# Performance work log

Hardware: AMD Instinct MI355X
Metric: run time of the kernel (lower is better)

## Reference

```python
import jax, jax.numpy as jnp
import numpy as np
import math

H, HKV, HD, HID = 32, 8, 128, 4096
ROPE_BASE = 10000.0

def rotate_half(x):
    x1, x2 = jnp.split(x, 2, axis=-1)
    return jnp.concatenate([-x2, x1], axis=-1)

def setup_inputs() -> dict:
    key = jax.random.key(0)
    ks = jax.random.split(key, 6)
    B, S = 1, 2048
    s = 0.02
    return {
        "hidden_states": jax.random.normal(ks[0], (B, S, HID), jnp.float32),
        "position_ids": jnp.arange(S, dtype=jnp.int64)[None, :].repeat(B, axis=0),
        # weights stored as [in, out] (transpose of torch Linear weight)
        "wq": jax.random.normal(ks[1], (HID, H * HD), jnp.float32) * s,
        "wk": jax.random.normal(ks[2], (HID, HKV * HD), jnp.float32) * s,
        "wv": jax.random.normal(ks[3], (HID, HKV * HD), jnp.float32) * s,
        "wo": jax.random.normal(ks[4], (H * HD, HID), jnp.float32) * s,
    }

def reference(hidden_states, position_ids, wq, wk, wv, wo):
    B, S, _ = hidden_states.shape
    g = H // HKV
    # projections
    q = (hidden_states @ wq).reshape(B, S, H, HD).transpose(0, 2, 1, 3)    # [B,H,S,D]
    k = (hidden_states @ wk).reshape(B, S, HKV, HD).transpose(0, 2, 1, 3)  # [B,Hkv,S,D]
    v = (hidden_states @ wv).reshape(B, S, HKV, HD).transpose(0, 2, 1, 3)
    # rotary embedding
    inv_freq = 1.0 / (ROPE_BASE ** (jnp.arange(0, HD, 2, dtype=jnp.float32) / HD))
    t = position_ids.astype(jnp.float32)                      # [B,S]
    freqs = t[..., None] * inv_freq[None, None, :]            # [B,S,D/2]
    emb = jnp.concatenate([freqs, freqs], axis=-1)            # [B,S,D]
    cos = jnp.cos(emb)[:, None, :, :]                         # [B,1,S,D]
    sin = jnp.sin(emb)[:, None, :, :]
    q = q * cos + rotate_half(q) * sin
    k = k * cos + rotate_half(k) * sin
    # GQA expansion (repeat_interleave over head dim)
    k = jnp.repeat(k, g, axis=1)                              # [B,H,S,D]
    v = jnpp_repeat(v, g) if False else jnp.repeat(v, g, axis=1)
    scale = 1.0 / math.sqrt(HD)
    scores = jnp.einsum('bhqd,bhkd->bhqk', q, k) * scale      # [B,H,S,S]
    causal = jnp.triu(jnp.full((S, S), -jnp.inf, jnp.float32), k=1)
    scores = scores + causal[None, None]
    attn = jax.nn.softmax(scores.astype(jnp.float32), axis=-1).astype(q.dtype)
    out = jnp.einsum('bhqk,bhkd->bhqd', attn, v)              # [B,H,S,D]
    out = out.transpose(0, 2, 1, 3).reshape(B, S, H * HD)
    return out @ wo
```

## Files before the change

### kernel.cpp

```cpp
#include <hip/hip_runtime.h>
#include <stdint.h>

#define DHEAD 128
#define DMODEL 4096
#define NQKV 6144
#define SEQLEN 2048

typedef __attribute__((ext_vector_type(8))) short bh8;
typedef __attribute__((ext_vector_type(4))) short bh4;
typedef __attribute__((ext_vector_type(4))) float f32x4;

__device__ __forceinline__ short f2bf(float f) {
  union { float f; unsigned u; } x; x.f = f;
  unsigned r = x.u + 0x7FFFu + ((x.u >> 16) & 1u);
  return (short)(r >> 16);
}
__device__ __forceinline__ float bf2f(short s) {
  union { unsigned u; float f; } x; x.u = ((unsigned)(unsigned short)s) << 16;
  return x.f;
}
__device__ __forceinline__ void async_cp16(const void* g, void* l) {
  __builtin_amdgcn_global_load_lds((const __attribute__((address_space(1))) void*)g,
                                   (__attribute__((address_space(3))) void*)l, 16, 0, 0);
}

#define BARRIER() do { asm volatile("" ::: "memory"); __builtin_amdgcn_s_barrier(); asm volatile("" ::: "memory"); } while (0)
#define LGKM0() asm volatile("s_waitcnt lgkmcnt(0)" ::: "memory")

__global__ void cvt_bf16_kernel(const float* __restrict__ src, short* __restrict__ dst, int n) {
  int idx = (blockIdx.x * blockDim.x + threadIdx.x) * 4;
  if (idx >= n) return;
  float4 v = *(const float4*)(src + idx);
  bh4 o;
  o.x = f2bf(v.x); o.y = f2bf(v.y); o.z = f2bf(v.z); o.w = f2bf(v.w);
  *(bh4*)(dst + idx) = o;
}

__global__ void cvt_t_kernel(const float* __restrict__ src, short* __restrict__ dst, int K, int N) {
  __shared__ float tile[32][33];
  int bx = blockIdx.x * 32;
  int by = blockIdx.y * 32;
  int tx = threadIdx.x, ty = threadIdx.y;
  for (int j = 0; j < 4; j++)
    tile[ty + 8 * j][tx] = src[(size_t)(by + ty + 8 * j) * N + bx + tx];
  __syncthreads();
  for (int j = 0; j < 4; j++)
    dst[(size_t)(bx + ty + 8 * j) * K + by + tx] = f2bf(tile[tx][ty + 8 * j]);
}

__global__ void vtrans_kernel(const short* __restrict__ qkv, short* __restrict__ VT) {
  __shared__ short tile[32][33];
  int bx = blockIdx.x * 32;
  int by = blockIdx.y * 32;
  int tx = threadIdx.x, ty = threadIdx.y;
  for (int j = 0; j < 4; j++)
    tile[ty + 8 * j][tx] = qkv[(size_t)(by + ty + 8 * j) * NQKV + 5120 + bx + tx];
  __syncthreads();
  for (int j = 0; j < 4; j++)
    VT[(size_t)(bx + ty + 8 * j) * 2048 + by + tx] = tile[tx][ty + 8 * j];
}

template <typename OutT>
__global__ __launch_bounds__(512, 2) void gemm256(const short* __restrict__ A, const short* __restrict__ Bt,
                                                  OutT* __restrict__ C, int M, int N, int K) {
  __shared__ __align__(16) short lds[2][2][256 * 64];
  const int tid = threadIdx.x;
  const int lane = tid & 63, w = tid >> 6;
  const int l15 = lane & 15, q4 = lane >> 4;
  const int m0 = blockIdx.y * 256, n0 = blockIdx.x * 256;
  const int wm = (w >> 2) * 128, wn = (w & 3) * 64;
  const int NT = K >> 6;

  char* const ldsBase = (char*)lds;

  const int srow = tid >> 3;
  const int scol = ((tid & 7) * 8) ^ ((tid & 32) ? 16 : 0);
  const short* const Asrc = A + (size_t)m0 * K + scol;
  const short* const Bsrc = Bt + (size_t)n0 * K + scol;

  auto stageA = [&](int buf, int h, int kt) {
    char* d = ldsBase + buf * 65536 + h * 16384 + tid * 16;
    const short* s = Asrc + (size_t)(h * 128 + srow) * K + kt * 64;
    async_cp16(s, d);
    async_cp16(s + (size_t)64 * K, d + 8192);
  };
  auto stageB = [&](int buf, int h, int kt) {
    char* d = ldsBase + buf * 65536 + 32768 + h * 16384 + tid * 16;
    const short* s = Bsrc + (size_t)(h * 128 + srow) * K + kt * 64;
    async_cp16(s, d);
    async_cp16(s + (size_t)64 * K, d + 8192);
  };

  const int flip = (l15 & 4) ? 32 : 0;
  const int rdA = (wm + l15) * 128;
  const int rdB = (wn + l15) * 128;
  const int rk0 = (q4 * 16) ^ flip;
  const int rk1 = (64 + q4 * 16) ^ flip;

  f32x4 acc[8][4] = {};
  bh8 af[4][2], bfr[4][2];

  stageA(0, 0, 0); stageA(0, 1, 0); stageB(0, 0, 0); stageB(0, 1, 0);
  stageB(1, 0, 1); stageB(1, 1, 1); stageA(1, 0, 1);
  asm volatile("s_waitcnt vmcnt(6)" ::: "memory");
  BARRIER();

  for (int t = 0; t < NT; ++t) {
    const int buf = t & 1;
    char* const Ar = ldsBase + buf * 65536;
    char* const Br = Ar + 32768;

#pragma unroll
    for (int i = 0; i < 4; i++) {
      af[i][0] = *(const bh8*)(Ar + rdA + i * 2048 + rk0);
      af[i][1] = *(const bh8*)(Ar + rdA + i * 2048 + rk1);
      bfr[i][0] = *(const bh8*)(Br + rdB + i * 2048 + rk0);
      bfr[i][1] = *(const bh8*)(Br + rdB + i * 2048 + rk1);
    }
    if (t + 1 < NT) stageA(buf ^ 1, 1, t + 1);
    BARRIER();
    LGKM0();
    __builtin_amdgcn_s_setprio(1);
#pragma unroll
    for (int i = 0; i < 4; i++)
#pragma unroll
      for (int j = 0; j < 2; j++) {
        acc[i][j] = __builtin_amdgcn_mfma_f32_16x16x32_bf16(af[i][0], bfr[j][0], acc[i][j], 0, 0, 0);
        acc[i][j] = __builtin_amdgcn_mfma_f32_16x16x32_bf16(af[i][1], bfr[j][1], acc[i][j], 0, 0, 0);
      }
    __builtin_amdgcn_s_setprio(0);
    BARRIER();

    if (t + 2 < NT) stageB(buf, 0, t + 2);
    BARRIER();
    __builtin_amdgcn_s_setprio(1);
#pragma unroll
    for (int i = 0; i < 4; i++)
#pragma unroll
      for (int j = 2; j < 4; j++) {
        acc[i][j] = __builtin_amdgcn_mfma_f32_16x16x32_bf16(af[i][0], bfr[j][0], acc[i][j], 0, 0, 0);
        acc[i][j] = __builtin_amdgcn_mfma_f32_16x16x32_bf16(af[i][1], bfr[j][1], acc[i][j], 0, 0, 0);
      }
    __builtin_amdgcn_s_setprio(0);
    BARRIER();

#pragma unroll
    for (int i = 0; i < 4; i++) {
      af[i][0] = *(const bh8*)(Ar + rdA + 8192 + i * 2048 + rk0);
      af[i][1] = *(const bh8*)(Ar + rdA + 8192 + i * 2048 + rk1);
    }
    if (t + 2 < NT) stageB(buf, 1, t + 2);
    BARRIER();
    LGKM0();
    __builtin_amdgcn_s_setprio(1);
#pragma unroll
    for (int i = 0; i < 4; i++)
#pragma unroll
      for (int j = 0; j < 2; j++) {
        acc[4 + i][j] = __builtin_amdgcn_mfma_f32_16x16x32_bf16(af[i][0], bfr[j][0], acc[4 + i][j], 0, 0, 0);
        acc[4 + i][j] = __builtin_amdgcn_mfma_f32_16x16x32_bf16(af[i][1], bfr[j][1], acc[4 + i][j], 0, 0, 0);
      }
    __builtin_amdgcn_s_setprio(0);
    BARRIER();

    if (t + 2 < NT) stageA(buf, 0, t + 2);
    BARRIER();
    __builtin_amdgcn_s_setprio(1);
#pragma unroll
    for (int i = 0; i < 4; i++)
#pragma unroll
      for (int j = 2; j < 4; j++) {
        acc[4 + i][j] = __builtin_amdgcn_mfma_f32_16x16x32_bf16(af[i][0], bfr[j][0], acc[4 + i][j], 0, 0, 0);
        acc[4 + i][j] = __builtin_amdgcn_mfma_f32_16x16x32_bf16(af[i][1], bfr[j][1], acc[4 + i][j], 0, 0, 0);
      }
    __builtin_amdgcn_s_setprio(0);
    if (t + 2 < NT)
      asm volatile("s_waitcnt vmcnt(6)" ::: "memory");
    else
      asm volatile("s_waitcnt vmcnt(0)" ::: "memory");
    BARRIER();
  }

#pragma unroll
  for (int i = 0; i < 8; i++)
#pragma unroll
    for (int j = 0; j < 4; j++)
#pragma unroll
      for (int r = 0; r < 4; r++) {
        int row = m0 + wm + i * 16 + q4 * 4 + r;
        int col = n0 + wn + j * 16 + l15;
        float v = acc[i][j][r];
        if constexpr (sizeof(OutT) == 2)
          ((short*)C)[(size_t)row * N + col] = f2bf(v);
        else
          C[(size_t)row * N + col] = v;
      }
}

__global__ void rope_kernel(short* __restrict__ qkv) {
  int idx = blockIdx.x * blockDim.x + threadIdx.x;
  int i = idx & 63;
  int slot = (idx >> 6) % 40;
  int row = idx / (40 * 64);
  short* p = qkv + (size_t)row * NQKV + (slot < 32 ? slot * DHEAD : 4096 + (slot - 32) * DHEAD) + i;
  float x1 = bf2f(p[0]), x2 = bf2f(p[64]);
  float inv = __expf((float)i * -0.14391156831212787f);
  float ang = (float)row * inv;
  float sn, cs;
  __sincosf(ang, &sn, &cs);
  p[0] = f2bf(x1 * cs - x2 * sn);
  p[64] = f2bf(x2 * cs + x1 * sn);
}

__global__ __launch_bounds__(256) void attn_kernel(const short* __restrict__ QKV, const short* __restrict__ VT,
                                                   short* __restrict__ O) {
  const int x = blockIdx.x;
  const int h = blockIdx.y;
  const int hkv = h >> 2;
  const int tid = threadIdx.x;
  const int lane = tid & 63, w = tid >> 6;
  const int l15 = lane & 15, q4 = lane >> 4;

  __shared__ __align__(16) short Kl[2][64 * 128];
  __shared__ __align__(16) short Vl[2][128 * 64];
  __shared__ __align__(16) short Pl[4][32 * 72];

  const bh8 ONES = {0x3F80, 0x3F80, 0x3F80, 0x3F80, 0x3F80, 0x3F80, 0x3F80, 0x3F80};
  const float SCL2 = 0.12751739343415342f;

  const int v_pb = (lane & 7) ^ ((lane >> 3) & 7);

  for (int phase = 0; phase < 2; phase++) {
    const int qt = phase == 0 ? (15 - x) : x;
    const int qb = qt * 128;
    const int n_kt = 2 * qt + 2;

    bh8 qf[2][4];
    for (int mi = 0; mi < 2; mi++) {
      const short* qp = QKV + (size_t)(qb + w * 32 + mi * 16 + l15) * NQKV + h * DHEAD + q4 * 8;
      for (int c = 0; c < 4; c++) qf[mi][c] = *(const bh8*)(qp + c * 32);
    }

    f32x4 O_acc[2][9] = {};

    __syncthreads();
    {
      const int kb = 0;
      for (int i = 0; i < 4; i++) {
        int r = w * 16 + i * 4 + q4;
        int db = l15 ^ (r & 15);
        async_cp16(QKV + (size_t)(kb + r) * NQKV + 4096 + hkv * DHEAD + db * 8,
                   (char*)&Kl[0][0] + (w * 256 + i * 64 + lane) * 16);
        int d = w * 32 + i * 8 + (lane >> 3);
        async_cp16(VT + (size_t)(hkv * DHEAD + d) * 2048 + kb + v_pb * 8,
                   (char*)&Vl[0][0] + (w * 256 + i * 64 + lane) * 16);
      }
    }

    for (int kt = 0; kt < n_kt; kt++) {
      const int p = kt & 1;
      const int kb = kt * 64;
      __syncthreads();
      if (kt + 1 < n_kt) {
        const int kb2 = kb + 64;
        for (int i = 0; i < 4; i++) {
          int r = w * 16 + i * 4 + q4;
          int db = l15 ^ (r & 15);
          async_cp16(QKV + (size_t)(kb2 + r) * NQKV + 4096 + hkv * DHEAD + db * 8,
                     (char*)&Kl[p ^ 1][0] + (w * 256 + i * 64 + lane) * 16);
          int d = w * 32 + i * 8 + (lane >> 3);
          async_cp16(VT + (size_t)(hkv * DHEAD + d) * 2048 + kb2 + v_pb * 8,
                     (char*)&Vl[p ^ 1][0] + (w * 256 + i * 64 + lane) * 16);
        }
      }

      const int row_base = qb + w * 32;
      const bool act0 = (kb <= row_base + 15);
      const bool act1 = (kb <= row_base + 31);
      if (act0 | act1) {
        for (int t = 0; t < 4; t++) {
          bh8 kf[4];
          for (int c = 0; c < 4; c++) {
            int sig = (c * 4 + q4) ^ l15;
            kf[c] = *(const bh8*)&Kl[p][(t * 16 + l15) * 128 + sig * 8];
          }
          for (int mi = 0; mi < 2; mi++) {
            if (!(mi ? act1 : act0)) continue;
            f32x4 a = {};
            for (int c = 0; c < 4; c++)
              a = __builtin_amdgcn_mfma_f32_16x16x32_bf16(qf[mi][c], kf[c], a, 0, 0, 0);
            int col = kb + t * 16 + l15;
            bool nm = (kb + 63 > row_base + mi * 16);
            for (int r = 0; r < 4; r++) {
              int row = row_base + mi * 16 + q4 * 4 + r;
              float pv = exp2f(a[r] * SCL2);
              if (nm && col > row) pv = 0.0f;
              Pl[w][(mi * 16 + q4 * 4 + r) * 72 + t * 16 + l15] = f2bf(pv);
            }
          }
        }

        for (int c = 0; c < 2; c++) {
          bh8 pf[2];
          if (act0) pf[0] = *(const bh8*)&Pl[w][(l15) * 72 + c * 32 + q4 * 8];
          if (act1) pf[1] = *(const bh8*)&Pl[w][(16 + l15) * 72 + c * 32 + q4 * 8];
          for (int n = 0; n < 8; n++) {
            int sig = (c * 4 + q4) ^ (l15 & 7);
            bh8 vf = *(const bh8*)&Vl[p][(n * 16 + l15) * 64 + sig * 8];
            if (act0) O_acc[0][n] = __builtin_amdgcn_mfma_f32_16x16x32_bf16(pf[0], vf, O_acc[0][n], 0, 0, 0);
            if (act1) O_acc[1][n] = __builtin_amdgcn_mfma_f32_16x16x32_bf16(pf[1], vf, O_acc[1][n], 0, 0, 0);
          }
          if (act0) O_acc[0][8] = __builtin_amdgcn_mfma_f32_16x16x32_bf16(pf[0], ONES, O_acc[0][8], 0, 0, 0);
          if (act1) O_acc[1][8] = __builtin_amdgcn_mfma_f32_16x16x32_bf16(pf[1], ONES, O_acc[1][8], 0, 0, 0);
        }
      }
    }

    for (int mi = 0; mi < 2; mi++)
      for (int r = 0; r < 4; r++) {
        float inv = 1.0f / O_acc[mi][8][r];
        int row = qb + w * 32 + mi * 16 + q4 * 4 + r;
        for (int n = 0; n < 8; n++) {
          int col = h * DHEAD + n * 16 + l15;
          O[(size_t)row * DMODEL + col] = f2bf(O_acc[mi][n][r] * inv);
        }
      }
  }
}

extern "C" void kernel_launch(void* const* d_in, const int* in_sizes, int n_in,
                              void* d_out, int out_size, void* d_ws, size_t ws_size,
                              hipStream_t stream) {
  const float* hs = (const float*)d_in[0];
  const float* wq = (const float*)d_in[2];
  const float* wk = (const float*)d_in[3];
  const float* wv = (const float*)d_in[4];
  const float* wo = (const float*)d_in[5];
  float* out = (float*)d_out;

  short* hsb = (short*)d_ws;
  short* wqkvT = hsb + (size_t)2048 * 4096;
  short* woT = wqkvT + (size_t)6144 * 4096;
  short* qkv = woT + (size_t)4096 * 4096;
  short* VT = qkv + (size_t)2048 * 6144;
  short* abuf = VT + (size_t)1024 * 2048;

  cvt_bf16_kernel<<<8192, 256, 0, stream>>>(hs, hsb, 2048 * 4096);
  cvt_t_kernel<<<dim3(128, 128), dim3(32, 8), 0, stream>>>(wq, wqkvT, 4096, 4096);
  cvt_t_kernel<<<dim3(32, 128), dim3(32, 8), 0, stream>>>(wk, wqkvT + (size_t)4096 * 4096, 4096, 1024);
  cvt_t_kernel<<<dim3(32, 128), dim3(32, 8), 0, stream>>>(wv, wqkvT + (size_t)5120 * 4096, 4096, 1024);
  cvt_t_kernel<<<dim3(128, 128), dim3(32, 8), 0, stream>>>(wo, woT, 4096, 4096);

  gemm256<short><<<dim3(24, 8), 512, 0, stream>>>(hsb, wqkvT, qkv, 2048, 6144, 4096);

  rope_kernel<<<20480, 256, 0, stream>>>(qkv);
  vtrans_kernel<<<dim3(32, 64), dim3(32, 8), 0, stream>>>(qkv, VT);

  attn_kernel<<<dim3(8, 32), 256, 0, stream>>>(qkv, VT, abuf);

  gemm256<float><<<dim3(16, 8), 512, 0, stream>>>(abuf, woT, out, 2048, 4096, 4096);
}
```

Before: 607.5 us.

## Use full XOR LDS swizzle in gemm256 and smaller-tile GEMM for output projection

Changes the LDS swizzle in gemm256 from a two-way flip to a full 8-way XOR of the 16-byte column chunk with the row index, on both the async store side and the fragment read side, to reduce LDS bank conflicts. Adds a simple 128x128 tile, single-buffered GEMM kernel and uses it for the output projection, giving 512 blocks instead of 128 for better CU occupancy. The new kernel has no double buffering and no swizzle, so it may expose load latency and bank conflicts.

```diff
diff --git a/kernel.cpp b/kernel.cpp
--- a/kernel.cpp
+++ b/kernel.cpp
@@ -61,6 +61,50 @@
 }
 
 template <typename OutT>
+__global__ __launch_bounds__(256) void gemm_bt(const short* __restrict__ A, const short* __restrict__ Bt,
+                                               OutT* __restrict__ C, int M, int N, int K) {
+  __shared__ __align__(16) short As[128 * 32];
+  __shared__ __align__(16) short Bs[128 * 32];
+  const int tid = threadIdx.x;
+  const int lane = tid & 63, w = tid >> 6;
+  const int l15 = lane & 15, q4 = lane >> 4;
+  const int m0 = blockIdx.y * 128, n0 = blockIdx.x * 128;
+  const int wm = (w >> 1) * 64, wn = (w & 1) * 64;
+
+  f32x4 acc[4][4] = {};
+
+  for (int k0 = 0; k0 < K; k0 += 32) {
+    for (int h = 0; h < 2; h++) {
+      int e = (h * 256 + tid) * 8;
+      int row = e >> 5, col = e & 31;
+      async_cp16(A + (size_t)(m0 + row) * K + k0 + col, &As[e]);
+      async_cp16(Bt + (size_t)(n0 + row) * K + k0 + col, &Bs[e]);
+    }
+    __syncthreads();
+    bh8 af[4], bf[4];
+    for (int t = 0; t < 4; t++) {
+      af[t] = *(const bh8*)&As[(wm + t * 16 + l15) * 32 + q4 * 8];
+      bf[t] = *(const bh8*)&Bs[(wn + t * 16 + l15) * 32 + q4 * 8];
+    }
+    for (int i = 0; i < 4; i++)
+      for (int j = 0; j < 4; j++)
+        acc[i][j] = __builtin_amdgcn_mfma_f32_16x16x32_bf16(af[i], bf[j], acc[i][j], 0, 0, 0);
+    __syncthreads();
+  }
+  for (int i = 0; i < 4; i++)
+    for (int j = 0; j < 4; j++)
+      for (int r = 0; r < 4; r++) {
+        int row = m0 + wm + i * 16 + q4 * 4 + r;
+        int col = n0 + wn + j * 16 + l15;
+        float v = acc[i][j][r];
+        if constexpr (sizeof(OutT) == 2)
+          ((short*)C)[(size_t)row * N + col] = f2bf(v);
+        else
+          C[(size_t)row * N + col] = v;
+      }
+}
+
+template <typename OutT>
 __global__ __launch_bounds__(512, 2) void gemm256(const short* __restrict__ A, const short* __restrict__ Bt,
                                                   OutT* __restrict__ C, int M, int N, int K) {
   __shared__ __align__(16) short lds[2][2][256 * 64];
@@ -74,7 +118,7 @@
   char* const ldsBase = (char*)lds;
 
   const int srow = tid >> 3;
-  const int scol = ((tid & 7) * 8) ^ ((tid & 32) ? 16 : 0);
+  const int scol = (((tid & 7) ^ (srow & 7)) * 8);
   const short* const Asrc = A + (size_t)m0 * K + scol;
   const short* const Bsrc = Bt + (size_t)n0 * K + scol;
 
@@ -91,7 +135,7 @@
     async_cp16(s + (size_t)64 * K, d + 8192);
   };
 
-  const int flip = (l15 & 4) ? 32 : 0;
+  const int flip = (l15 & 7) << 4;
   const int rdA = (wm + l15) * 128;
   const int rdB = (wn + l15) * 128;
   const int rk0 = (q4 * 16) ^ flip;
@@ -358,5 +402,5 @@
 
   attn_kernel<<<dim3(8, 32), 256, 0, stream>>>(qkv, VT, abuf);
 
-  gemm256<float><<<dim3(16, 8), 512, 0, stream>>>(abuf, woT, out, 2048, 4096, 4096);
-}
+  gemm_bt<float><<<dim3(32, 16), 256, 0, stream>>>(abuf, woT, out, 2048, 4096, 4096);
+}
```

Measured after the change: 563.9 us. -7.2%, faster.

## Retile QKV GEMM to 192-wide tiles and split-K the output projection

Applied to the files above, without the earlier changes.

The QKV projection gets a new 256x192-tile GEMM kernel, so the grid has 256 blocks instead of 192 and fills more compute units. The output projection GEMM is split along K into two halves with blockIdx.z. Each half writes fp32 partials into the reused workspace, and a new elementwise add kernel sums them. The LDS swizzle in both GEMMs becomes a full 8-way XOR pattern to reduce bank conflicts. The split-K path costs extra fp32 partial traffic and one extra kernel launch.

```diff
diff --git a/kernel.cpp b/kernel.cpp
--- a/kernel.cpp
+++ b/kernel.cpp
@@ -34,6 +34,17 @@
   bh4 o;
   o.x = f2bf(v.x); o.y = f2bf(v.y); o.z = f2bf(v.z); o.w = f2bf(v.w);
   *(bh4*)(dst + idx) = o;
+}
+
+__global__ void add2_f32(const float* __restrict__ a, const float* __restrict__ b,
+                         float* __restrict__ o, int n) {
+  int i = (blockIdx.x * blockDim.x + threadIdx.x) * 4;
+  if (i >= n) return;
+  float4 x = *(const float4*)(a + i);
+  float4 y = *(const float4*)(b + i);
+  float4 z;
+  z.x = x.x + y.x; z.y = x.y + y.y; z.z = x.z + y.z; z.w = x.w + y.w;
+  *(float4*)(o + i) = z;
 }
 
 __global__ void cvt_t_kernel(const float* __restrict__ src, short* __restrict__ dst, int K, int N) {
@@ -60,9 +71,155 @@
     VT[(size_t)(bx + ty + 8 * j) * 2048 + by + tx] = tile[tx][ty + 8 * j];
 }
 
+__global__ __launch_bounds__(512, 2) void gemm192(const short* __restrict__ A, const short* __restrict__ Bt,
+                                                  short* __restrict__ C, int M, int N, int K) {
+  __shared__ __align__(16) char lds[2 * 57344];
+  const int tid = threadIdx.x;
+  const int lane = tid & 63, w = tid >> 6;
+  const int l15 = lane & 15, q4 = lane >> 4;
+  const int m0 = blockIdx.y * 256, n0 = blockIdx.x * 192;
+  const int wm = (w >> 2) * 128, wn = (w & 3) * 48;
+  const int NT = K >> 6;
+  char* const ldsBase = lds;
+
+  const int srow = tid >> 3;
+  const int scol = (((tid & 7) ^ (srow & 7)) * 8);
+  const short* const Asrc = A + (size_t)m0 * K + scol;
+  const short* const Bsrc = Bt + (size_t)n0 * K + scol;
+
+  auto stageA = [&](int buf, int h, int kt) {
+    char* d = ldsBase + buf * 57344 + h * 16384 + tid * 16;
+    const short* s = Asrc + (size_t)(h * 128 + srow) * K + kt * 64;
+    async_cp16(s, d);
+    async_cp16(s + (size_t)64 * K, d + 8192);
+  };
+  auto stageB = [&](int buf, int third, int kt) {
+    char* d = ldsBase + buf * 57344 + 32768 + third * 8192 + tid * 16;
+    const short* s = Bsrc + (size_t)(third * 64 + srow) * K + kt * 64;
+    async_cp16(s, d);
+  };
+
+  const int flip = (l15 & 7) << 4;
+  const int rdA = (wm + l15) * 128;
+  const int rdB = (wn + l15) * 128;
+  const int rk0 = (q4 * 16) ^ flip;
+  const int rk1 = (64 + q4 * 16) ^ flip;
+
+  f32x4 acc[8][3] = {};
+  bh8 af[2][2], bfr[3][2];
+
+  stageA(0, 0, 0); stageA(0, 1, 0);
+  stageB(0, 0, 0); stageB(0, 1, 0); stageB(0, 2, 0);
+  stageB(1, 0, 1); stageB(1, 1, 1); stageB(1, 2, 1);
+  asm volatile("s_waitcnt vmcnt(3)" ::: "memory");
+  BARRIER();
+
+  for (int t = 0; t < NT; ++t) {
+    const int buf = t & 1;
+    char* const Ar = ldsBase + buf * 57344;
+    char* const Br = Ar + 32768;
+
+#pragma unroll
+    for (int ii = 0; ii < 2; ii++) {
+      af[ii][0] = *(const bh8*)(Ar + rdA + ii * 2048 + rk0);
+      af[ii][1] = *(const bh8*)(Ar + rdA + ii * 2048 + rk1);
+    }
+#pragma unroll
+    for (int j = 0; j < 3; j++) {
+      bfr[j][0] = *(const bh8*)(Br + rdB + j * 2048 + rk0);
+      bfr[j][1] = *(const bh8*)(Br + rdB + j * 2048 + rk1);
+    }
+    if (t + 1 < NT) stageA(buf ^ 1, 1, t + 1);
+    BARRIER();
+    LGKM0();
+    __builtin_amdgcn_s_setprio(1);
+#pragma unroll
+    for (int ii = 0; ii < 2; ii++)
+#pragma unroll
+      for (int j = 0; j < 3; j++) {
+        acc[ii][j] = __builtin_amdgcn_mfma_f32_16x16x32_bf16(af[ii][0], bfr[j][0], acc[ii][j], 0, 0, 0);
+        acc[ii][j] = __builtin_amdgcn_mfma_f32_16x16x32_bf16(af[ii][1], bfr[j][1], acc[ii][j], 0, 0, 0);
+      }
+    __builtin_amdgcn_s_setprio(0);
+    BARRIER();
+
+#pragma unroll
+    for (int ii = 0; ii < 2; ii++) {
+      af[ii][0] = *(const bh8*)(Ar + rdA + (2 + ii) * 2048 + rk0);
+      af[ii][1] = *(const bh8*)(Ar + rdA + (2 + ii) * 2048 + rk1);
+    }
+    if (t + 1 < NT) stageA(buf ^ 1, 0, t + 1);
+    BARRIER();
+    LGKM0();
+    __builtin_amdgcn_s_setprio(1);
+#pragma unroll
+    for (int ii = 0; ii < 2; ii++)
+#pragma unroll
+      for (int j = 0; j < 3; j++) {
+        acc[2 + ii][j] = __builtin_amdgcn_mfma_f32_16x16x32_bf16(af[ii][0], bfr[j][0], acc[2 + ii][j], 0, 0, 0);
+        acc[2 + ii][j] = __builtin_amdgcn_mfma_f32_16x16x32_bf16(af[ii][1], bfr[j][1], acc[2 + ii][j], 0, 0, 0);
+      }
+    __builtin_amdgcn_s_setprio(0);
+    BARRIER();
+
+#pragma unroll
+    for (int ii = 0; ii < 2; ii++) {
+      af[ii][0] = *(const bh8*)(Ar + rdA + (4 + ii) * 2048 + rk0);
+      af[ii][1] = *(const bh8*)(Ar + rdA + (4 + ii) * 2048 + rk1);
+    }
+    if (t + 2 < NT) { stageB(buf, 0, t + 2); stageB(buf, 1, t + 2); }
+    BARRIER();
+    LGKM0();
+    __builtin_amdgcn_s_setprio(1);
+#pragma unroll
+    for (int ii = 0; ii < 2; ii++)
+#pragma unroll
+      for (int j = 0; j < 3; j++) {
+        acc[4 + ii][j] = __builtin_amdgcn_mfma_f32_16x16x32_bf16(af[ii][0], bfr[j][0], acc[4 + ii][j], 0, 0, 0);
+        acc[4 + ii][j] = __builtin_amdgcn_mfma_f32_16x16x32_bf16(af[ii][1], bfr[j][1], acc[4 + ii][j], 0, 0, 0);
+      }
+    __builtin_amdgcn_s_setprio(0);
+    BARRIER();
+
+#pragma unroll
+    for (int ii = 0; ii < 2; ii++) {
+      af[ii][0] = *(const bh8*)(Ar + rdA + (6 + ii) * 2048 + rk0);
+      af[ii][1] = *(const bh8*)(Ar + rdA + (6 + ii) * 2048 + rk1);
+    }
+    if (t + 2 < NT) stageB(buf, 2, t + 2);
+    BARRIER();
+    LGKM0();
+    __builtin_amdgcn_s_setprio(1);
+#pragma unroll
+    for (int ii = 0; ii < 2; ii++)
+#pragma unroll
+      for (int j = 0; j < 3; j++) {
+        acc[6 + ii][j] = __builtin_amdgcn_mfma_f32_16x16x32_bf16(af[ii][0], bfr[j][0], acc[6 + ii][j], 0, 0, 0);
+        acc[6 + ii][j] = __builtin_amdgcn_mfma_f32_16x16x32_bf16(af[ii][1], bfr[j][1], acc[6 + ii][j], 0, 0, 0);
+      }
+    __builtin_amdgcn_s_setprio(0);
+    if (t + 2 < NT)
+      asm volatile("s_waitcnt vmcnt(3)" ::: "memory");
+    else
+      asm volatile("s_waitcnt vmcnt(0)" ::: "memory");
+    BARRIER();
+  }
+
+#pragma unroll
+  for (int i = 0; i < 8; i++)
+#pragma unroll
+    for (int j = 0; j < 3; j++)
+#pragma unroll
+      for (int r = 0; r < 4; r++) {
+        int row = m0 + wm + i * 16 + q4 * 4 + r;
+        int col = n0 + wn + j * 16 + l15;
+        C[(size_t)row * N + col] = f2bf(acc[i][j][r]);
+      }
+}
+
 template <typename OutT>
 __global__ __launch_bounds__(512, 2) void gemm256(const short* __restrict__ A, const short* __restrict__ Bt,
-                                                  OutT* __restrict__ C, int M, int N, int K) {
+                                                  OutT* __restrict__ C, int M, int N, int K, int LDK) {
   __shared__ __align__(16) short lds[2][2][256 * 64];
   const int tid = threadIdx.x;
   const int lane = tid & 63, w = tid >> 6;
@@ -71,27 +228,30 @@
   const int wm = (w >> 2) * 128, wn = (w & 3) * 64;
   const int NT = K >> 6;
 
+  const size_t zk = (size_t)blockIdx.z * K;
+  OutT* const Cz = C + (size_t)blockIdx.z * M * N;
+
   char* const ldsBase = (char*)lds;
 
   const int srow = tid >> 3;
-  const int scol = ((tid & 7) * 8) ^ ((tid & 32) ? 16 : 0);
-  const short* const Asrc = A + (size_t)m0 * K + scol;
-  const short* const Bsrc = Bt + (size_t)n0 * K + scol;
+  const int scol = (((tid & 7) ^ (srow & 7)) * 8);
+  const short* const Asrc = A + (size_t)m0 * LDK + zk + scol;
+  const short* const Bsrc = Bt + (size_t)n0 * LDK + zk + scol;
 
   auto stageA = [&](int buf, int h, int kt) {
     char* d = ldsBase + buf * 65536 + h * 16384 + tid * 16;
-    const short* s = Asrc + (size_t)(h * 128 + srow) * K + kt * 64;
+    const short* s = Asrc + (size_t)(h * 128 + srow) * LDK + kt * 64;
     async_cp16(s, d);
-    async_cp16(s + (size_t)64 * K, d + 8192);
+    async_cp16(s + (size_t)64 * LDK, d + 8192);
   };
   auto stageB = [&](int buf, int h, int kt) {
     char* d = ldsBase + buf * 65536 + 32768 + h * 16384 + tid * 16;
-    const short* s = Bsrc + (size_t)(h * 128 + srow) * K + kt * 64;
+    const short* s = Bsrc + (size_t)(h * 128 + srow) * LDK + kt * 64;
     async_cp16(s, d);
-    async_cp16(s + (size_t)64 * K, d + 8192);
+    async_cp16(s + (size_t)64 * LDK, d + 8192);
   };
 
-  const int flip = (l15 & 4) ? 32 : 0;
+  const int flip = (l15 & 7) << 4;
   const int rdA = (wm + l15) * 128;
   const int rdB = (wn + l15) * 128;
   const int rk0 = (q4 * 16) ^ flip;
@@ -191,9 +351,9 @@
         int col = n0 + wn + j * 16 + l15;
         float v = acc[i][j][r];
         if constexpr (sizeof(OutT) == 2)
-          ((short*)C)[(size_t)row * N + col] = f2bf(v);
+          ((short*)Cz)[(size_t)row * N + col] = f2bf(v);
         else
-          C[(size_t)row * N + col] = v;
+          Cz[(size_t)row * N + col] = v;
       }
 }
 
@@ -344,6 +504,7 @@
   short* qkv = woT + (size_t)4096 * 4096;
   short* VT = qkv + (size_t)2048 * 6144;
   short* abuf = VT + (size_t)1024 * 2048;
+  float* p01 = (float*)d_ws;
 
   cvt_bf16_kernel<<<8192, 256, 0, stream>>>(hs, hsb, 2048 * 4096);
   cvt_t_kernel<<<dim3(128, 128), dim3(32, 8), 0, stream>>>(wq, wqkvT, 4096, 4096);
@@ -351,12 +512,13 @@
   cvt_t_kernel<<<dim3(32, 128), dim3(32, 8), 0, stream>>>(wv, wqkvT + (size_t)5120 * 4096, 4096, 1024);
   cvt_t_kernel<<<dim3(128, 128), dim3(32, 8), 0, stream>>>(wo, woT, 4096, 4096);
 
-  gemm256<short><<<dim3(24, 8), 512, 0, stream>>>(hsb, wqkvT, qkv, 2048, 6144, 4096);
+  gemm192<<<dim3(32, 8), 512, 0, stream>>>(hsb, wqkvT, qkv, 2048, 6144, 4096);
 
   rope_kernel<<<20480, 256, 0, stream>>>(qkv);
   vtrans_kernel<<<dim3(32, 64), dim3(32, 8), 0, stream>>>(qkv, VT);
 
   attn_kernel<<<dim3(8, 32), 256, 0, stream>>>(qkv, VT, abuf);
 
-  gemm256<float><<<dim3(16, 8), 512, 0, stream>>>(abuf, woT, out, 2048, 4096, 4096);
-}
+  gemm256<float><<<dim3(16, 8, 2), 512, 0, stream>>>(abuf, woT, p01, 2048, 4096, 2048, 4096);
+  add2_f32<<<8192, 256, 0, stream>>>(p01, p01 + (size_t)2048 * 4096, out, 2048 * 4096);
+}
```

After: 526.7 us. 13.3% less time.
